# Optimization experiments

Hardware: AMD Instinct MI355X
Metric: run time of the kernel (lower is better)

Reference implementation:

```python
import jax, jax.numpy as jnp
import numpy as np

N = 50000   # nodes
E = 800000  # edges
D = 128     # input feature dim
H = 128     # hidden dim
L = 3       # num GIN layers
G = 64      # graphs in batch


def setup_inputs() -> dict:
    key = jax.random.key(0)
    ks = jax.random.split(key, 20)
    inp = {
        "h": jax.random.normal(ks[0], (N, D), jnp.float32),
        "src": jax.random.randint(ks[1], (E,), 0, N),
        "dst": jax.random.randint(ks[2], (E,), 0, N),
        "graph_ids": jnp.sort(jax.random.randint(ks[3], (N,), 0, G)),
    }
    k = 4
    for i in range(L):
        in_dim = D if i == 0 else H
        inp[f"w1_{i}"] = jax.random.normal(ks[k], (in_dim, H), jnp.float32) / np.sqrt(in_dim).astype(np.float32); k += 1
        inp[f"b1_{i}"] = jnp.zeros((H,), jnp.float32)
        inp[f"w2_{i}"] = jax.random.normal(ks[k], (H, H), jnp.float32) / np.sqrt(H).astype(np.float32); k += 1
        inp[f"b2_{i}"] = jnp.zeros((H,), jnp.float32)
    inp["w_out"] = jax.random.normal(ks[k], (H * L, 1), jnp.float32) / np.sqrt(H * L).astype(np.float32)
    inp["b_out"] = jnp.zeros((1,), jnp.float32)
    return inp


def _gin_layer(h, src, dst, w1, b1, w2, b2):
    # sum aggregation over edges: agg[i] = sum_{(j->i) in E} h[j]
    agg = jax.ops.segment_sum(h[src], dst, num_segments=N)
    z = h + agg  # (1 + eps) * h + agg with eps = 0 (DGL GINConv default)
    return jax.nn.relu(z @ w1 + b1) @ w2 + b2  # 2-layer MLP


def reference(h, src, dst, graph_ids,
              w1_0, b1_0, w2_0, b2_0,
              w1_1, b1_1, w2_1, b2_1,
              w1_2, b1_2, w2_2, b2_2,
              w_out, b_out):
    layers = [(w1_0, b1_0, w2_0, b2_0),
              (w1_1, b1_1, w2_1, b2_1),
              (w1_2, b1_2, w2_2, b2_2)]
    readouts = []
    for w1, b1, w2, b2 in layers:
        h = _gin_layer(h, src, dst, w1, b1, w2, b2)
        # per-graph sum readout of node features: [G, H]
        readouts.append(jax.ops.segment_sum(h, graph_ids, num_segments=G))
    hg = jnp.concatenate(readouts, axis=1)  # [G, H*L]
    return hg @ w_out + b_out  # [G, 1]
```

## Files before the change

### kernel.cpp

```cpp
#include <hip/hip_runtime.h>

#define NN 50000
#define NE 800000
#define DIMH 128
#define NGRAPH 64
#define NTILES 3125
#define PAIRS 1024
#define MLP_BLOCKS 512
#define MLP_ITERS 4
#define NBIN 196
#define BCAP 8064
#define SL_US 800000
#define SL_U2 200000

typedef __attribute__((ext_vector_type(8))) short bf16x8;
typedef __attribute__((ext_vector_type(4))) float f32x4;

__device__ __forceinline__ unsigned short f2b(float f) {
  unsigned int b = __float_as_uint(f);
  unsigned int r = (b + 0x7FFFu + ((b >> 16) & 1u)) >> 16;
  return (unsigned short)r;
}
__device__ __forceinline__ float b2f_lo(unsigned int u) { return __uint_as_float(u << 16); }
__device__ __forceinline__ float b2f_hi(unsigned int u) { return __uint_as_float(u & 0xffff0000u); }
__device__ __forceinline__ unsigned int pk2(float lo, float hi) {
  return (unsigned int)f2b(lo) | ((unsigned int)f2b(hi) << 16);
}


__global__ __launch_bounds__(256) void bin_scatter_kernel(const int* __restrict__ src,
                                                          const int* __restrict__ dst,
                                                          int* __restrict__ gcnt,
                                                          int2* __restrict__ staging) {
  __shared__ int hist[NBIN];
  __shared__ int base[NBIN];
  int tid = threadIdx.x;
  for (int i = tid; i < NBIN; i += 256) hist[i] = 0;
  __syncthreads();
  int e0 = blockIdx.x * 2048;
  int2 ed[8];
  int bin[8], rank[8];
#pragma unroll
  for (int k = 0; k < 8; ++k) {
    int e = e0 + k * 256 + tid;
    bin[k] = 0; rank[k] = 0; ed[k] = make_int2(0, 0);
    if (e < NE) {
      ed[k].x = src[e]; ed[k].y = dst[e];
      bin[k] = ed[k].y >> 8;
      rank[k] = atomicAdd(&hist[bin[k]], 1);
    }
  }
  __syncthreads();
  for (int i = tid; i < NBIN; i += 256) base[i] = atomicAdd(&gcnt[i], hist[i]);
  __syncthreads();
#pragma unroll
  for (int k = 0; k < 8; ++k) {
    int e = e0 + k * 256 + tid;
    if (e < NE) staging[bin[k] * BCAP + base[bin[k]] + rank[k]] = ed[k];
  }
}

__global__ __launch_bounds__(256) void bin_fill_kernel(const int2* __restrict__ staging,
                                                       const int* __restrict__ gcnt,
                                                       int* __restrict__ adj,
                                                       int* __restrict__ row_ptr,
                                                       int* __restrict__ cnt,
                                                       int* __restrict__ alloc) {
  __shared__ int hdeg[256], loc[256], c2[256];
  __shared__ int sbase;
  int b = blockIdx.x;
  int tid = threadIdx.x;
  hdeg[tid] = 0; c2[tid] = 0;
  __syncthreads();
  int n = gcnt[b];
  for (int i = tid; i < n; i += 256)
    atomicAdd(&hdeg[staging[b * BCAP + i].y & 255], 1);
  __syncthreads();
  int v = hdeg[tid];
  loc[tid] = v;
  __syncthreads();
  for (int off = 1; off < 256; off <<= 1) {
    int t = (tid >= off) ? loc[tid - off] : 0;
    __syncthreads();
    loc[tid] += t;
    __syncthreads();
  }
  if (tid == 255) sbase = atomicAdd(alloc, loc[255]);
  __syncthreads();
  int excl = loc[tid] - v;
  int node = b * 256 + tid;
  if (node < NN) { row_ptr[node] = sbase + excl; cnt[node] = v; }
  loc[tid] = excl;
  __syncthreads();
  for (int i = tid; i < n; i += 256) {
    int2 e = staging[b * BCAP + i];
    int local = e.y & 255;
    int r = atomicAdd(&c2[local], 1);
    adj[sbase + loc[local] + r] = e.x;
  }
}


struct WPtrs { const float* w[6]; const float* b_out; };

__global__ __launch_bounds__(256) void prep_kernel(WPtrs ptrs, unsigned short* __restrict__ wt,
                                                   float* __restrict__ out,
                                                   int* __restrict__ gcnt,
                                                   int* __restrict__ alloc) {
  int i = blockIdx.x * 256 + threadIdx.x;
  int m = i >> 14;
  int idx = i & 16383;
  int c = idx >> 7, k = idx & 127;
  wt[m * 16384 + idx] = f2b(ptrs.w[m][k * DIMH + c]);
  if (i < NGRAPH) out[i] = ptrs.b_out[0];
  if (i < NBIN) gcnt[i] = 0;
  if (i == NBIN) *alloc = 0;
}

__global__ void convh_kernel(const float* __restrict__ h, uint2* __restrict__ Hs) {
  int t = blockIdx.x * 256 + threadIdx.x;
  int node = t >> 5;
  int q = t & 31;
  float4 v = *(const float4*)&h[node * DIMH + q * 4];
  uint2 o;
  o.x = pk2(v.x, v.y);
  o.y = pk2(v.z, v.w);
  Hs[(q >> 2) * SL_U2 + node * 4 + (q & 3)] = o;
}

__global__ __launch_bounds__(256) void agg_kernel(const uint2* __restrict__ Hs,
                                                  const int* __restrict__ row_ptr,
                                                  const int* __restrict__ cnt,
                                                  const int* __restrict__ adj,
                                                  uint2* __restrict__ Zs) {
  int bid = blockIdx.x;
  int slice = bid & 7;
  int nb = bid >> 3;
  int tid = threadIdx.x;
  int node = nb * 64 + (tid >> 2);
  int l4 = tid & 3;
  if (node >= NN) return;
  const uint2* hp = Hs + slice * SL_U2;
  int start = row_ptr[node];
  int c = cnt[node];
  uint2 own = hp[node * 4 + l4];
  float a0 = b2f_lo(own.x), a1 = b2f_hi(own.x), a2 = b2f_lo(own.y), a3 = b2f_hi(own.y);
  int j = 0;
  for (; j + 4 <= c; j += 4) {
    int my = adj[start + j + l4];
    int n0 = __shfl(my, 0, 4), n1 = __shfl(my, 1, 4);
    int n2 = __shfl(my, 2, 4), n3 = __shfl(my, 3, 4);
    uint2 u0 = hp[n0 * 4 + l4], u1 = hp[n1 * 4 + l4];
    uint2 u2 = hp[n2 * 4 + l4], u3 = hp[n3 * 4 + l4];
    a0 += b2f_lo(u0.x); a1 += b2f_hi(u0.x); a2 += b2f_lo(u0.y); a3 += b2f_hi(u0.y);
    a0 += b2f_lo(u1.x); a1 += b2f_hi(u1.x); a2 += b2f_lo(u1.y); a3 += b2f_hi(u1.y);
    a0 += b2f_lo(u2.x); a1 += b2f_hi(u2.x); a2 += b2f_lo(u2.y); a3 += b2f_hi(u2.y);
    a0 += b2f_lo(u3.x); a1 += b2f_hi(u3.x); a2 += b2f_lo(u3.y); a3 += b2f_hi(u3.y);
  }
  for (; j < c; ++j) {
    int nbr = adj[start + j];
    uint2 u = hp[nbr * 4 + l4];
    a0 += b2f_lo(u.x); a1 += b2f_hi(u.x); a2 += b2f_lo(u.y); a3 += b2f_hi(u.y);
  }
  uint2 o;
  o.x = pk2(a0, a1);
  o.y = pk2(a2, a3);
  Zs[slice * SL_U2 + node * 4 + l4] = o;
}

__global__ __launch_bounds__(256, 2) void mlp_kernel(const unsigned short* __restrict__ X,
                                                     const unsigned short* __restrict__ W1t,
                                                     const float* __restrict__ b1,
                                                     const unsigned short* __restrict__ W2t,
                                                     const float* __restrict__ b2,
                                                     unsigned short* __restrict__ Y,
                                                     const int* __restrict__ gids,
                                                     const float* __restrict__ wout,
                                                     float* __restrict__ gout) {
  __shared__ unsigned short y1[2][2][2048];
  __shared__ float s_gout[NGRAPH];
  int tid = threadIdx.x;
  if (tid < NGRAPH) s_gout[tid] = 0.f;

  int wv = tid >> 6;
  int lane = tid & 63;
  int pb = wv >> 1;
  int half = wv & 1;
  int l15 = lane & 15;
  int g = lane >> 4;
  int p = blockIdx.x * 2 + pb;

  int asl_base = (g >> 1) * SL_US + (g & 1) * 8 + l15 * 16;

  bf16x8 a[4];
  {
    int roff = p * 256;
#pragma unroll
    for (int kt = 0; kt < 4; ++kt)
      a[kt] = *(const bf16x8*)(X + 2 * kt * SL_US + roff + asl_base);
  }

  bf16x8 fb1[4][4], fb2[4][4];
  const unsigned short* w1b = W1t + (half * 64 + l15) * DIMH + g * 8;
  const unsigned short* w2b = W2t + (half * 64 + l15) * DIMH + g * 8;
#pragma unroll
  for (int n = 0; n < 4; ++n)
#pragma unroll
    for (int kt = 0; kt < 4; ++kt) {
      fb1[n][kt] = *(const bf16x8*)(w1b + n * 16 * DIMH + kt * 32);
      fb2[n][kt] = *(const bf16x8*)(w2b + n * 16 * DIMH + kt * 32);
    }
  float b1v[4], b2v[4], wov[4];
#pragma unroll
  for (int n = 0; n < 4; ++n) {
    int col = half * 64 + n * 16 + l15;
    b1v[n] = b1[col];
    b2v[n] = b2[col];
    wov[n] = wout[col];
  }
  __syncthreads();

#pragma unroll
  for (int i = 0; i < MLP_ITERS; ++i) {
    int rtc = p + i * PAIRS;
    bool active = rtc < NTILES;
    unsigned short* buf = y1[pb][i & 1];

    if (active) {
#pragma unroll
      for (int n = 0; n < 4; ++n) {
        f32x4 acc = (f32x4){0.f, 0.f, 0.f, 0.f};
#pragma unroll
        for (int kt = 0; kt < 4; ++kt)
          acc = __builtin_amdgcn_mfma_f32_16x16x32_bf16(a[kt], fb1[n][kt], acc, 0, 0, 0);
        int col2 = (half * 64 + n * 16 + l15) * 2;
#pragma unroll
        for (int r = 0; r < 4; ++r) {
          float f = fmaxf(acc[r] + b1v[n], 0.f);
          int row = 4 * g + r;
          buf[((row * 256 + col2) ^ (row << 4)) >> 1] = f2b(f);
        }
      }
    }

    int rtn = p + (i + 1) * PAIRS;
    if (i + 1 < MLP_ITERS && rtn < NTILES) {
      int roff = rtn * 256;
#pragma unroll
      for (int kt = 0; kt < 4; ++kt)
        a[kt] = *(const bf16x8*)(X + 2 * kt * SL_US + roff + asl_base);
    }

    __syncthreads();

    if (active) {
      bf16x8 a2[4];
#pragma unroll
      for (int kt = 0; kt < 4; ++kt)
        a2[kt] = *(const bf16x8*)&buf[((l15 * 256 + kt * 64 + g * 16) ^ (l15 << 4)) >> 1];

      float pr[4] = {0.f, 0.f, 0.f, 0.f};
#pragma unroll
      for (int n = 0; n < 4; ++n) {
        f32x4 acc = (f32x4){0.f, 0.f, 0.f, 0.f};
#pragma unroll
        for (int kt = 0; kt < 4; ++kt)
          acc = __builtin_amdgcn_mfma_f32_16x16x32_bf16(a2[kt], fb2[n][kt], acc, 0, 0, 0);
        int sl = 4 * half + n;
#pragma unroll
        for (int r = 0; r < 4; ++r) {
          float f = acc[r] + b2v[n];
          if (Y) Y[sl * SL_US + (rtc * 16 + 4 * g + r) * 16 + l15] = f2b(f);
          pr[r] += f * wov[n];
        }
      }
#pragma unroll
      for (int r = 0; r < 4; ++r) {
#pragma unroll
        for (int off = 1; off < 16; off <<= 1) pr[r] += __shfl_xor(pr[r], off, 64);
      }
      if (l15 == 0) {
#pragma unroll
        for (int r = 0; r < 4; ++r)
          atomicAdd(&s_gout[gids[rtc * 16 + 4 * g + r]], pr[r]);
      }
    }
  }

  __syncthreads();
  if (tid < NGRAPH) {
    float v = s_gout[tid];
    if (v != 0.f) atomicAdd(&gout[tid], v);
  }
}


extern "C" void kernel_launch(void* const* d_in, const int* in_sizes, int n_in,
                              void* d_out, int out_size, void* d_ws, size_t ws_size,
                              hipStream_t stream) {
  const float* h = (const float*)d_in[0];
  const int* src = (const int*)d_in[1];
  const int* dst = (const int*)d_in[2];
  const int* gids = (const int*)d_in[3];
  const float* w_out = (const float*)d_in[16];
  const float* b_out = (const float*)d_in[17];
  float* out = (float*)d_out;

  char* base = (char*)d_ws;
  unsigned short* buf0 = (unsigned short*)(base);
  unsigned short* buf1 = (unsigned short*)(base + 12800000);
  int2* staging = (int2*)(base + 25600000);
  int* adj = (int*)(base + 38400000);
  int* row_ptr = (int*)(base + 41600000);
  int* cnt = (int*)(base + 41800064);
  int* gcnt = (int*)(base + 42000128);
  int* alloc = (int*)(base + 42001024);
  unsigned short* wt = (unsigned short*)(base + 42002048);

  WPtrs ptrs;
  for (int l = 0; l < 3; ++l) {
    ptrs.w[2 * l] = (const float*)d_in[4 + l * 4];
    ptrs.w[2 * l + 1] = (const float*)d_in[6 + l * 4];
  }
  ptrs.b_out = b_out;

  prep_kernel<<<384, 256, 0, stream>>>(ptrs, wt, out, gcnt, alloc);
  bin_scatter_kernel<<<(NE + 2047) / 2048, 256, 0, stream>>>(src, dst, gcnt, staging);
  bin_fill_kernel<<<NBIN, 256, 0, stream>>>(staging, gcnt, adj, row_ptr, cnt, alloc);
  convh_kernel<<<(NN * 32) / 256 + 1, 256, 0, stream>>>(h, (uint2*)buf0);

  int agg_blocks = 782 * 8;

  for (int l = 0; l < 3; ++l) {
    const float* b1 = (const float*)d_in[5 + l * 4];
    const float* b2 = (const float*)d_in[7 + l * 4];
    const unsigned short* Hl = (l & 1) ? buf1 : buf0;
    unsigned short* Yl = (l & 1) ? buf0 : buf1;
    unsigned short* Zl = (unsigned short*)staging;
    Zl = (unsigned short*)(base + 42300000);
    agg_kernel<<<agg_blocks, 256, 0, stream>>>((const uint2*)Hl, row_ptr, cnt, adj,
                                               (uint2*)Zl);
    mlp_kernel<<<MLP_BLOCKS, 256, 0, stream>>>(Zl, wt + (2 * l) * 16384, b1,
                                               wt + (2 * l + 1) * 16384, b2,
                                               (l == 2) ? nullptr : Yl,
                                               gids, w_out + l * DIMH, out);
  }
}
```

Before: 225.1 us.

## Fold last-layer W2 into readout vector and widen aggregation gathers to 16 bytes

For the last GIN layer, precomputes v2 = W2·w_out and s2 = b2·w_out in the prep kernel, so the final MLP skips the second matmul and the Y store and reduces the ReLU output against v2 directly. The aggregation kernel now has two lanes per node, each gathering 16-byte uint4 chunks, and reads neighbor indices as int2 pairs with an 8-way unrolled loop. To make those int2 index loads aligned, adjacency rows are padded to even length. The risks are extra memory traffic from the padding and fewer threads in flight per node, which lowers gather parallelism, plus a small change in rounding order from the algebraic fold.

```diff
diff --git a/kernel.cpp b/kernel.cpp
--- a/kernel.cpp
+++ b/kernel.cpp
@@ -11,7 +11,7 @@
 #define NBIN 196
 #define BCAP 8064
 #define SL_US 800000
-#define SL_U2 200000
+#define SL_U4 100000
 
 typedef __attribute__((ext_vector_type(8))) short bf16x8;
 typedef __attribute__((ext_vector_type(4))) float f32x4;
@@ -25,6 +25,12 @@
 __device__ __forceinline__ float b2f_hi(unsigned int u) { return __uint_as_float(u & 0xffff0000u); }
 __device__ __forceinline__ unsigned int pk2(float lo, float hi) {
   return (unsigned int)f2b(lo) | ((unsigned int)f2b(hi) << 16);
+}
+__device__ __forceinline__ void add8(float* a, uint4 u) {
+  a[0] += b2f_lo(u.x); a[1] += b2f_hi(u.x);
+  a[2] += b2f_lo(u.y); a[3] += b2f_hi(u.y);
+  a[4] += b2f_lo(u.z); a[5] += b2f_hi(u.z);
+  a[6] += b2f_lo(u.w); a[7] += b2f_hi(u.w);
 }
 
 
@@ -77,7 +83,8 @@
     atomicAdd(&hdeg[staging[b * BCAP + i].y & 255], 1);
   __syncthreads();
   int v = hdeg[tid];
-  loc[tid] = v;
+  int va = (v + 1) & ~1;
+  loc[tid] = va;
   __syncthreads();
   for (int off = 1; off < 256; off <<= 1) {
     int t = (tid >= off) ? loc[tid - off] : 0;
@@ -87,7 +94,7 @@
   }
   if (tid == 255) sbase = atomicAdd(alloc, loc[255]);
   __syncthreads();
-  int excl = loc[tid] - v;
+  int excl = loc[tid] - va;
   int node = b * 256 + tid;
   if (node < NN) { row_ptr[node] = sbase + excl; cnt[node] = v; }
   loc[tid] = excl;
@@ -101,12 +108,15 @@
 }
 
 
-struct WPtrs { const float* w[6]; const float* b_out; };
+struct WPtrs { const float* w[6]; const float* b_out; const float* b2_last;
+               const float* w_out; };
 
 __global__ __launch_bounds__(256) void prep_kernel(WPtrs ptrs, unsigned short* __restrict__ wt,
                                                    float* __restrict__ out,
                                                    int* __restrict__ gcnt,
-                                                   int* __restrict__ alloc) {
+                                                   int* __restrict__ alloc,
+                                                   float* __restrict__ v2,
+                                                   float* __restrict__ s2) {
   int i = blockIdx.x * 256 + threadIdx.x;
   int m = i >> 14;
   int idx = i & 16383;
@@ -115,57 +125,87 @@
   if (i < NGRAPH) out[i] = ptrs.b_out[0];
   if (i < NBIN) gcnt[i] = 0;
   if (i == NBIN) *alloc = 0;
+  if (i < DIMH) {
+    float s = 0.f;
+    const float* w2r = ptrs.w[5] + i * DIMH;
+    for (int cc = 0; cc < DIMH; ++cc) s += w2r[cc] * ptrs.w_out[2 * DIMH + cc];
+    v2[i] = s;
+  }
+  if (i == DIMH) {
+    float s = 0.f;
+    for (int cc = 0; cc < DIMH; ++cc) s += ptrs.b2_last[cc] * ptrs.w_out[2 * DIMH + cc];
+    *s2 = s;
+  }
 }
 
 __global__ void convh_kernel(const float* __restrict__ h, uint2* __restrict__ Hs) {
   int t = blockIdx.x * 256 + threadIdx.x;
+  if (t >= NN * 32) return;
   int node = t >> 5;
   int q = t & 31;
   float4 v = *(const float4*)&h[node * DIMH + q * 4];
   uint2 o;
   o.x = pk2(v.x, v.y);
   o.y = pk2(v.z, v.w);
-  Hs[(q >> 2) * SL_U2 + node * 4 + (q & 3)] = o;
-}
-
-__global__ __launch_bounds__(256) void agg_kernel(const uint2* __restrict__ Hs,
+  Hs[(q >> 2) * (SL_U4 * 2) + node * 4 + (q & 3)] = o;
+}
+
+__global__ __launch_bounds__(256) void agg_kernel(const uint4* __restrict__ Hs,
                                                   const int* __restrict__ row_ptr,
                                                   const int* __restrict__ cnt,
                                                   const int* __restrict__ adj,
-                                                  uint2* __restrict__ Zs) {
+                                                  uint4* __restrict__ Zs) {
   int bid = blockIdx.x;
   int slice = bid & 7;
   int nb = bid >> 3;
   int tid = threadIdx.x;
-  int node = nb * 64 + (tid >> 2);
-  int l4 = tid & 3;
+  int node = nb * 128 + (tid >> 1);
+  int l2 = tid & 1;
   if (node >= NN) return;
-  const uint2* hp = Hs + slice * SL_U2;
+  const uint4* hp = Hs + slice * SL_U4;
   int start = row_ptr[node];
   int c = cnt[node];
-  uint2 own = hp[node * 4 + l4];
-  float a0 = b2f_lo(own.x), a1 = b2f_hi(own.x), a2 = b2f_lo(own.y), a3 = b2f_hi(own.y);
+  float a[8];
+  {
+    uint4 own = hp[node * 2 + l2];
+    a[0] = b2f_lo(own.x); a[1] = b2f_hi(own.x);
+    a[2] = b2f_lo(own.y); a[3] = b2f_hi(own.y);
+    a[4] = b2f_lo(own.z); a[5] = b2f_hi(own.z);
+    a[6] = b2f_lo(own.w); a[7] = b2f_hi(own.w);
+  }
   int j = 0;
-  for (; j + 4 <= c; j += 4) {
-    int my = adj[start + j + l4];
-    int n0 = __shfl(my, 0, 4), n1 = __shfl(my, 1, 4);
-    int n2 = __shfl(my, 2, 4), n3 = __shfl(my, 3, 4);
-    uint2 u0 = hp[n0 * 4 + l4], u1 = hp[n1 * 4 + l4];
-    uint2 u2 = hp[n2 * 4 + l4], u3 = hp[n3 * 4 + l4];
-    a0 += b2f_lo(u0.x); a1 += b2f_hi(u0.x); a2 += b2f_lo(u0.y); a3 += b2f_hi(u0.y);
-    a0 += b2f_lo(u1.x); a1 += b2f_hi(u1.x); a2 += b2f_lo(u1.y); a3 += b2f_hi(u1.y);
-    a0 += b2f_lo(u2.x); a1 += b2f_hi(u2.x); a2 += b2f_lo(u2.y); a3 += b2f_hi(u2.y);
-    a0 += b2f_lo(u3.x); a1 += b2f_hi(u3.x); a2 += b2f_lo(u3.y); a3 += b2f_hi(u3.y);
-  }
-  for (; j < c; ++j) {
-    int nbr = adj[start + j];
-    uint2 u = hp[nbr * 4 + l4];
-    a0 += b2f_lo(u.x); a1 += b2f_hi(u.x); a2 += b2f_lo(u.y); a3 += b2f_hi(u.y);
-  }
-  uint2 o;
-  o.x = pk2(a0, a1);
-  o.y = pk2(a2, a3);
-  Zs[slice * SL_U2 + node * 4 + l4] = o;
+  for (; j + 8 <= c; j += 8) {
+    int2 i01 = *(const int2*)(adj + start + j);
+    int2 i23 = *(const int2*)(adj + start + j + 2);
+    int2 i45 = *(const int2*)(adj + start + j + 4);
+    int2 i67 = *(const int2*)(adj + start + j + 6);
+    uint4 u0 = hp[i01.x * 2 + l2];
+    uint4 u1 = hp[i01.y * 2 + l2];
+    uint4 u2 = hp[i23.x * 2 + l2];
+    uint4 u3 = hp[i23.y * 2 + l2];
+    uint4 u4 = hp[i45.x * 2 + l2];
+    uint4 u5 = hp[i45.y * 2 + l2];
+    uint4 u6 = hp[i67.x * 2 + l2];
+    uint4 u7 = hp[i67.y * 2 + l2];
+    add8(a, u0); add8(a, u1); add8(a, u2); add8(a, u3);
+    add8(a, u4); add8(a, u5); add8(a, u6); add8(a, u7);
+  }
+  for (; j + 2 <= c; j += 2) {
+    int2 i01 = *(const int2*)(adj + start + j);
+    uint4 u0 = hp[i01.x * 2 + l2];
+    uint4 u1 = hp[i01.y * 2 + l2];
+    add8(a, u0); add8(a, u1);
+  }
+  if (j < c) {
+    int n0 = adj[start + j];
+    add8(a, hp[n0 * 2 + l2]);
+  }
+  uint4 o;
+  o.x = pk2(a[0], a[1]);
+  o.y = pk2(a[2], a[3]);
+  o.z = pk2(a[4], a[5]);
+  o.w = pk2(a[6], a[7]);
+  Zs[slice * SL_U4 + node * 2 + l2] = o;
 }
 
 __global__ __launch_bounds__(256, 2) void mlp_kernel(const unsigned short* __restrict__ X,
@@ -176,11 +216,14 @@
                                                      unsigned short* __restrict__ Y,
                                                      const int* __restrict__ gids,
                                                      const float* __restrict__ wout,
-                                                     float* __restrict__ gout) {
+                                                     float* __restrict__ gout,
+                                                     const float* __restrict__ v2,
+                                                     const float* __restrict__ s2p) {
   __shared__ unsigned short y1[2][2][2048];
   __shared__ float s_gout[NGRAPH];
   int tid = threadIdx.x;
   if (tid < NGRAPH) s_gout[tid] = 0.f;
+  bool last = (v2 != nullptr);
 
   int wv = tid >> 6;
   int lane = tid & 63;
@@ -208,15 +251,17 @@
 #pragma unroll
     for (int kt = 0; kt < 4; ++kt) {
       fb1[n][kt] = *(const bf16x8*)(w1b + n * 16 * DIMH + kt * 32);
-      fb2[n][kt] = *(const bf16x8*)(w2b + n * 16 * DIMH + kt * 32);
+      if (!last) fb2[n][kt] = *(const bf16x8*)(w2b + n * 16 * DIMH + kt * 32);
     }
-  float b1v[4], b2v[4], wov[4];
+  float b1v[4], b2v[4], wov[4], v2v[4];
+  float s2v = last ? *s2p : 0.f;
 #pragma unroll
   for (int n = 0; n < 4; ++n) {
     int col = half * 64 + n * 16 + l15;
     b1v[n] = b1[col];
-    b2v[n] = b2[col];
-    wov[n] = wout[col];
+    b2v[n] = last ? 0.f : b2[col];
+    wov[n] = last ? 0.f : wout[col];
+    v2v[n] = last ? v2[col] : 0.f;
   }
   __syncthreads();
 
@@ -227,6 +272,7 @@
     unsigned short* buf = y1[pb][i & 1];
 
     if (active) {
+      float pr1[4] = {0.f, 0.f, 0.f, 0.f};
 #pragma unroll
       for (int n = 0; n < 4; ++n) {
         f32x4 acc = (f32x4){0.f, 0.f, 0.f, 0.f};
@@ -237,8 +283,25 @@
 #pragma unroll
         for (int r = 0; r < 4; ++r) {
           float f = fmaxf(acc[r] + b1v[n], 0.f);
-          int row = 4 * g + r;
-          buf[((row * 256 + col2) ^ (row << 4)) >> 1] = f2b(f);
+          if (!last) {
+            int row = 4 * g + r;
+            buf[((row * 256 + col2) ^ (row << 4)) >> 1] = f2b(f);
+          } else {
+            pr1[r] += f * v2v[n];
+          }
+        }
+      }
+      if (last) {
+#pragma unroll
+        for (int r = 0; r < 4; ++r) {
+#pragma unroll
+          for (int off = 1; off < 16; off <<= 1) pr1[r] += __shfl_xor(pr1[r], off, 64);
+        }
+        if (l15 == 0) {
+          float s2add = (half == 0) ? s2v : 0.f;
+#pragma unroll
+          for (int r = 0; r < 4; ++r)
+            atomicAdd(&s_gout[gids[rtc * 16 + 4 * g + r]], pr1[r] + s2add);
         }
       }
     }
@@ -253,7 +316,7 @@
 
     __syncthreads();
 
-    if (active) {
+    if (active && !last) {
       bf16x8 a2[4];
 #pragma unroll
       for (int kt = 0; kt < 4; ++kt)
@@ -270,7 +333,7 @@
 #pragma unroll
         for (int r = 0; r < 4; ++r) {
           float f = acc[r] + b2v[n];
-          if (Y) Y[sl * SL_US + (rtc * 16 + 4 * g + r) * 16 + l15] = f2b(f);
+          Y[sl * SL_US + (rtc * 16 + 4 * g + r) * 16 + l15] = f2b(f);
           pr[r] += f * wov[n];
         }
       }
@@ -311,11 +374,14 @@
   unsigned short* buf1 = (unsigned short*)(base + 12800000);
   int2* staging = (int2*)(base + 25600000);
   int* adj = (int*)(base + 38400000);
-  int* row_ptr = (int*)(base + 41600000);
-  int* cnt = (int*)(base + 41800064);
-  int* gcnt = (int*)(base + 42000128);
-  int* alloc = (int*)(base + 42001024);
-  unsigned short* wt = (unsigned short*)(base + 42002048);
+  int* row_ptr = (int*)(base + 41800064);
+  int* cnt = (int*)(base + 42000128);
+  int* gcnt = (int*)(base + 42200192);
+  int* alloc = (int*)(base + 42201024);
+  unsigned short* wt = (unsigned short*)(base + 42201088);
+  float* v2 = (float*)(base + 42397696);
+  float* s2 = (float*)(base + 42398208);
+  unsigned short* Zs = (unsigned short*)(base + 42400000);
 
   WPtrs ptrs;
   for (int l = 0; l < 3; ++l) {
@@ -323,26 +389,29 @@
     ptrs.w[2 * l + 1] = (const float*)d_in[6 + l * 4];
   }
   ptrs.b_out = b_out;
-
-  prep_kernel<<<384, 256, 0, stream>>>(ptrs, wt, out, gcnt, alloc);
+  ptrs.b2_last = (const float*)d_in[15];
+  ptrs.w_out = w_out;
+
+  prep_kernel<<<384, 256, 0, stream>>>(ptrs, wt, out, gcnt, alloc, v2, s2);
   bin_scatter_kernel<<<(NE + 2047) / 2048, 256, 0, stream>>>(src, dst, gcnt, staging);
   bin_fill_kernel<<<NBIN, 256, 0, stream>>>(staging, gcnt, adj, row_ptr, cnt, alloc);
-  convh_kernel<<<(NN * 32) / 256 + 1, 256, 0, stream>>>(h, (uint2*)buf0);
-
-  int agg_blocks = 782 * 8;
+  convh_kernel<<<(NN * 32 + 255) / 256, 256, 0, stream>>>(h, (uint2*)buf0);
+
+  int agg_blocks = 391 * 8;
 
   for (int l = 0; l < 3; ++l) {
     const float* b1 = (const float*)d_in[5 + l * 4];
     const float* b2 = (const float*)d_in[7 + l * 4];
     const unsigned short* Hl = (l & 1) ? buf1 : buf0;
     unsigned short* Yl = (l & 1) ? buf0 : buf1;
-    unsigned short* Zl = (unsigned short*)staging;
-    Zl = (unsigned short*)(base + 42300000);
-    agg_kernel<<<agg_blocks, 256, 0, stream>>>((const uint2*)Hl, row_ptr, cnt, adj,
-                                               (uint2*)Zl);
-    mlp_kernel<<<MLP_BLOCKS, 256, 0, stream>>>(Zl, wt + (2 * l) * 16384, b1,
+    int lastl = (l == 2);
+    agg_kernel<<<agg_blocks, 256, 0, stream>>>((const uint4*)Hl, row_ptr, cnt, adj,
+                                               (uint4*)Zs);
+    mlp_kernel<<<MLP_BLOCKS, 256, 0, stream>>>(Zs, wt + (2 * l) * 16384, b1,
                                                wt + (2 * l + 1) * 16384, b2,
-                                               (l == 2) ? nullptr : Yl,
-                                               gids, w_out + l * DIMH, out);
-  }
-}
+                                               lastl ? nullptr : Yl,
+                                               gids, w_out + l * DIMH, out,
+                                               lastl ? v2 : nullptr,
+                                               lastl ? s2 : nullptr);
+  }
+}
```

Result: faster. 220.6 us (-2.0%).
